# Optimization experiments

Measured on AMD Instinct MI355X. Metric: run time of the kernel, lower is better.

Reference implementation:

```python
import jax, jax.numpy as jnp
import numpy as np

B, CIN, H, W = 16, 512, 64, 64
CP = 256  # planes
G = 8     # groups
EPS = 1e-5


def setup_inputs() -> dict:
    key = jax.random.key(0)
    ks = jax.random.split(key, 7)
    s_in = 1.0 / np.sqrt(CIN)
    s_zp = 1.0 / np.sqrt(CP // G)
    return {
        "x": jax.random.normal(ks[0], (B, CIN, H, W), dtype=jnp.float32),
        "Wt": jax.random.uniform(ks[1], (CP, CIN), jnp.float32, -s_in, s_in),
        "Wp": jax.random.uniform(ks[2], (CP, CIN), jnp.float32, -s_in, s_in),
        "Wg": jax.random.uniform(ks[3], (CP, CIN), jnp.float32, -s_in, s_in),
        # grouped 1x1 conv z: (groups, out_per_group=CIN//G, in_per_group=CP//G)
        "Wz": jax.random.uniform(ks[4], (G, CIN // G, CP // G), jnp.float32, -s_zp, s_zp),
        "gamma": jnp.ones((CIN,), jnp.float32),
        "beta": jnp.zeros((CIN,), jnp.float32),
    }


def reference(x, Wt, Wp, Wg, Wz, gamma, beta):
    b, cin, h, w = x.shape
    cp = Wt.shape[0]
    cg = cp // G  # channels per group in bottleneck
    n = cg * h * w

    # 1x1 convs == channel matmuls
    t = jnp.einsum("oi,bihw->bohw", Wt, x)
    p = jnp.einsum("oi,bihw->bohw", Wp, x)
    g = jnp.einsum("oi,bihw->bohw", Wg, x)

    # per-group CGNL dot-product kernel: att = <p_g, g_g> (scalar), y = att * t_g
    t = t.reshape(b, G, n)
    p = p.reshape(b, G, n)
    g = g.reshape(b, G, n)
    att = jnp.sum(p * g, axis=-1, keepdims=True)  # (b, G, 1); use_scale=False
    y = (att * t).reshape(b, G, cg, h * w)

    # grouped 1x1 conv z back to cin channels
    z = jnp.einsum("goc,bgcn->bgon", Wz, y).reshape(b, cin, h, w)

    # GroupNorm(G, cin) + residual
    zr = z.reshape(b, G, (cin // G) * h * w)
    mu = jnp.mean(zr, axis=-1, keepdims=True)
    var = jnp.var(zr, axis=-1, keepdims=True)
    zn = ((zr - mu) * jax.lax.rsqrt(var + EPS)).reshape(b, cin, h, w)
    out = zn * gamma[None, :, None, None] + beta[None, :, None, None] + x
    return out
```

## Files before the change

### kernel.cpp

```cpp
#include <hip/hip_runtime.h>
#include <stddef.h>
#include <stdint.h>

#define B_   16
#define CIN_ 512
#define HW_  4096
#define CP_  256
#define G_   8
#define EPS_ 1e-5f

typedef _Float16 f16;
typedef _Float16 f16x8 __attribute__((ext_vector_type(8)));
typedef _Float16 f16x2 __attribute__((ext_vector_type(2)));
typedef float    f32x4 __attribute__((ext_vector_type(4)));

#define OFF_WALL   0u
#define OFF_WZH    786432u
#define OFF_ATT    819200u
#define OFF_STATS  819712u
#define OFF_T      1048576u
#define OFF_XH     34603008u

#if defined(__has_builtin)
#if __has_builtin(__builtin_amdgcn_fdot2)
#define HAVE_FDOT2 1
#endif
#endif

__device__ __forceinline__ float dot2acc(f16x2 a, f16x2 b, float c) {
#ifdef HAVE_FDOT2
  return __builtin_amdgcn_fdot2(a, b, c, false);
#else
  return fmaf((float)a[0], (float)b[0], fmaf((float)a[1], (float)b[1], c));
#endif
}

__global__ __launch_bounds__(256) void k_prep0(
    const float* __restrict__ Wt, const float* __restrict__ Wp,
    const float* __restrict__ Wg, const float* __restrict__ Wz,
    char* __restrict__ ws)
{
  f16*   wall  = (f16*)(ws + OFF_WALL);
  f16*   wzh   = (f16*)(ws + OFF_WZH);
  float* att   = (float*)(ws + OFF_ATT);
  int idx = blockIdx.x * 256 + threadIdx.x;
  if (idx < 768 * 512) {
    int r = idx >> 9, k = idx & 511;
    float v;
    if (r < 256) v = Wt[r * 512 + k];
    else {
      int q = r - 256, o = q >> 1;
      v = (q & 1) ? Wg[o * 512 + k] : Wp[o * 512 + k];
    }
    wall[idx] = (f16)v;
  } else if (idx < 768 * 512 + 16384) {
    int i = idx - 768 * 512;
    wzh[i] = (f16)Wz[i];
  } else if (idx < 768 * 512 + 16384 + 384) {
    att[idx - (768 * 512 + 16384)] = 0.f;
  }
}

__global__ __launch_bounds__(256) void k_xpose(const float* __restrict__ x,
                                               f16* __restrict__ xh)
{
  __shared__ f16 T[64][72];
  const int tid = threadIdx.x;
  const int c0  = blockIdx.x * 64;
  const int hw0 = blockIdx.y * 64;
  const int b   = blockIdx.z;

  const int cr  = (tid >> 4) * 4;
  const int hwr = (tid & 15) * 4;
  const float* xb = x + ((size_t)b * CIN_ + c0) * HW_ + hw0;

  float4 v[4];
#pragma unroll
  for (int j = 0; j < 4; j++)
    v[j] = *(const float4*)(xb + (size_t)(cr + j) * HW_ + hwr);

#pragma unroll
  for (int i = 0; i < 4; i++) {
    f16 pk[4];
#pragma unroll
    for (int j = 0; j < 4; j++) pk[j] = (f16)((const float*)&v[j])[i];
    *(f16x2*)&T[hwr + i][cr]     = f16x2{pk[0], pk[1]};
    *(f16x2*)&T[hwr + i][cr + 2] = f16x2{pk[2], pk[3]};
  }
  __syncthreads();

  const int hwo = tid >> 2;
  const int cb  = (tid & 3) * 16;
  f16* dst = xh + ((size_t)b * HW_ + hw0 + hwo) * 512 + c0 + cb;
  *(f16x8*)(dst)     = *(const f16x8*)&T[hwo][cb];
  *(f16x8*)(dst + 8) = *(const f16x8*)&T[hwo][cb + 8];
}

__global__ __launch_bounds__(256) void k_gemm(
    const f16* __restrict__ xh, const f16* __restrict__ wall,
    f16* __restrict__ tbuf, float* __restrict__ att, int bchunk)
{
  __shared__ f16 As[128 * 64];
  __shared__ f16 Bs[128 * 64];

  const int tid = threadIdx.x;
  const int bid = blockIdx.x;
  const int logical = (bid & 7) * 96 + (bid >> 3);
  const int nt = logical % 6;
  const int mt = (logical / 6) & 31;
  const int bl = logical / 192;
  const int M0 = mt * 128;
  const int N0 = nt * 128;

  const int l  = tid & 63;
  const int w  = tid >> 6;
  const int wy = w >> 1, wx = w & 1;

  const f16* xb = xh + (size_t)bl * HW_ * 512;

  f32x4 acc[4][4] = {};

  const int srow  = tid >> 3;
  const int sslot = tid & 7;
  const unsigned ldsW = (unsigned)(w * 1024);

  for (int k0 = 0; k0 < 512; k0 += 64) {
    __syncthreads();
#pragma unroll
    for (int i = 0; i < 4; i++) {
      const int r  = srow + i * 32;
      const int sl = sslot ^ (r & 7);
      const f16* ga = xb + (size_t)(M0 + r) * 512 + k0 + sl * 8;
      __builtin_amdgcn_global_load_lds(
          (const __attribute__((address_space(1))) void*)ga,
          (__attribute__((address_space(3))) void*)((char*)As + i * 4096 + ldsW),
          16, 0, 0);
      const f16* gb = wall + (size_t)(N0 + r) * 512 + k0 + sl * 8;
      __builtin_amdgcn_global_load_lds(
          (const __attribute__((address_space(1))) void*)gb,
          (__attribute__((address_space(3))) void*)((char*)Bs + i * 4096 + ldsW),
          16, 0, 0);
    }
    __syncthreads();

#pragma unroll
    for (int ks = 0; ks < 2; ks++) {
      f16x8 af[4], bf[4];
#pragma unroll
      for (int f = 0; f < 4; f++) {
        const int ra = wy * 64 + f * 16 + (l & 15);
        const int sa = (ks * 4 + (l >> 4)) ^ (ra & 7);
        af[f] = *(const f16x8*)&As[ra * 64 + sa * 8];
        const int rb = wx * 64 + f * 16 + (l & 15);
        const int sb = (ks * 4 + (l >> 4)) ^ (rb & 7);
        bf[f] = *(const f16x8*)&Bs[rb * 64 + sb * 8];
      }
#pragma unroll
      for (int fi = 0; fi < 4; fi++)
#pragma unroll
        for (int fj = 0; fj < 4; fj++)
          acc[fi][fj] = __builtin_amdgcn_mfma_f32_16x16x32_f16(
              af[fi], bf[fj], acc[fi][fj], 0, 0, 0);
    }
  }

  const int bg = bchunk + bl;
  if (N0 < 256) {
    f16* tb = tbuf + (size_t)bg * HW_ * 256;
#pragma unroll
    for (int fi = 0; fi < 4; fi++) {
      const int hwr = M0 + wy * 64 + fi * 16 + (l >> 4) * 4;
#pragma unroll
      for (int fj = 0; fj < 4; fj++) {
        const int c = N0 + wx * 64 + fj * 16 + (l & 15);
#pragma unroll
        for (int r = 0; r < 4; r++)
          tb[(size_t)(hwr + r) * 256 + c] = (f16)acc[fi][fj][r];
      }
    }
  } else {
    float s = 0.f;
#pragma unroll
    for (int fi = 0; fi < 4; fi++)
#pragma unroll
      for (int fj = 0; fj < 4; fj++)
#pragma unroll
        for (int r = 0; r < 4; r++) {
          const float v = acc[fi][fj][r];
          s += v * __shfl_xor(v, 1);
        }
#pragma unroll
    for (int off = 32; off > 0; off >>= 1) s += __shfl_xor(s, off);
    if (l == 0) {
      const int grp = (N0 + wx * 64 - 256) >> 6;
      atomicAdd(&att[bg * G_ + grp], 0.5f * s);
    }
  }
}

__global__ __launch_bounds__(256) void k_stats(
    const f16* __restrict__ tbuf, const f16* __restrict__ wzh,
    float* __restrict__ stats)
{
  __shared__ f16x2 wzs[64 * 16];
  __shared__ float red[8];
  const int tid = threadIdx.x;
  const int n0 = blockIdx.x * 1024;
  const int g  = blockIdx.y;
  const int b  = blockIdx.z;

  ((uint4*)wzs)[tid] = ((const uint4*)(wzh + (size_t)g * 2048))[tid];
  __syncthreads();

  const f16* tb = tbuf + ((size_t)b * HW_ + n0 + tid * 4) * 256 + g * 32;
  f16x8 tv[4][4];
#pragma unroll
  for (int j = 0; j < 4; j++)
#pragma unroll
    for (int q = 0; q < 4; q++)
      tv[j][q] = *(const f16x8*)(tb + (size_t)j * 256 + q * 8);

  float s1 = 0.f, s2 = 0.f;
#pragma unroll 2
  for (int o = 0; o < 64; o++) {
    float u[4] = {0.f, 0.f, 0.f, 0.f};
#pragma unroll
    for (int q = 0; q < 4; q++) {
#pragma unroll
      for (int e = 0; e < 4; e++) {
        const f16x2 wz2 = wzs[o * 16 + q * 4 + e];
#pragma unroll
        for (int j = 0; j < 4; j++) {
          const f16x2 t2 = {tv[j][q][2 * e], tv[j][q][2 * e + 1]};
          u[j] = dot2acc(wz2, t2, u[j]);
        }
      }
    }
#pragma unroll
    for (int j = 0; j < 4; j++) {
      s1 += u[j];
      s2 = fmaf(u[j], u[j], s2);
    }
  }
#pragma unroll
  for (int off = 32; off > 0; off >>= 1) {
    s1 += __shfl_xor(s1, off);
    s2 += __shfl_xor(s2, off);
  }
  if ((tid & 63) == 0) { red[(tid >> 6) * 2] = s1; red[(tid >> 6) * 2 + 1] = s2; }
  __syncthreads();
  if (tid == 0) {
    atomicAdd(&stats[(b * G_ + g) * 2 + 0], red[0] + red[2] + red[4] + red[6]);
    atomicAdd(&stats[(b * G_ + g) * 2 + 1], red[1] + red[3] + red[5] + red[7]);
  }
}

__global__ __launch_bounds__(256) void k_out(
    const f16* __restrict__ tbuf, const f16* __restrict__ wzh,
    const float* __restrict__ x, const float* __restrict__ gamma,
    const float* __restrict__ beta, const float* __restrict__ att,
    const float* __restrict__ stats, float* __restrict__ out)
{
  __shared__ f16x2 wzs[64 * 16];
  const int tid = threadIdx.x;
  const int n0 = blockIdx.x * 1024;
  const int g  = blockIdx.y;
  const int b  = blockIdx.z;

  ((uint4*)wzs)[tid] = ((const uint4*)(wzh + (size_t)g * 2048))[tid];
  __syncthreads();

  const f16* tb = tbuf + ((size_t)b * HW_ + n0 + tid * 4) * 256 + g * 32;
  f16x8 tv[4][4];
#pragma unroll
  for (int j = 0; j < 4; j++)
#pragma unroll
    for (int q = 0; q < 4; q++)
      tv[j][q] = *(const f16x8*)(tb + (size_t)j * 256 + q * 8);

  const float attv = att[b * G_ + g];
  const float invN = 1.f / (64.f * 4096.f);
  const float S1 = stats[(b * G_ + g) * 2 + 0];
  const float S2 = stats[(b * G_ + g) * 2 + 1];
  const float mu  = S1 * invN;
  const float var = S2 * invN - mu * mu;
  const float sc  = attv * rsqrtf(attv * attv * var + EPS_);

#pragma unroll 2
  for (int o = 0; o < 64; o++) {
    float u[4] = {0.f, 0.f, 0.f, 0.f};
#pragma unroll
    for (int q = 0; q < 4; q++) {
#pragma unroll
      for (int e = 0; e < 4; e++) {
        const f16x2 wz2 = wzs[o * 16 + q * 4 + e];
#pragma unroll
        for (int j = 0; j < 4; j++) {
          const f16x2 t2 = {tv[j][q][2 * e], tv[j][q][2 * e + 1]};
          u[j] = dot2acc(wz2, t2, u[j]);
        }
      }
    }
    const int c = g * 64 + o;
    const float gm = gamma[c];
    const float bt = beta[c];
    const size_t off = ((size_t)b * CIN_ + c) * HW_ + n0 + tid * 4;
    const float4 xv = *(const float4*)(x + off);
    float4 ov;
    ov.x = fmaf((u[0] - mu) * sc, gm, bt + xv.x);
    ov.y = fmaf((u[1] - mu) * sc, gm, bt + xv.y);
    ov.z = fmaf((u[2] - mu) * sc, gm, bt + xv.z);
    ov.w = fmaf((u[3] - mu) * sc, gm, bt + xv.w);
    *(float4*)(out + off) = ov;
  }
}

extern "C" void kernel_launch(void* const* d_in, const int* in_sizes, int n_in,
                              void* d_out, int out_size, void* d_ws, size_t ws_size,
                              hipStream_t stream)
{
  const float* x     = (const float*)d_in[0];
  const float* Wt    = (const float*)d_in[1];
  const float* Wp    = (const float*)d_in[2];
  const float* Wg    = (const float*)d_in[3];
  const float* Wz    = (const float*)d_in[4];
  const float* gamma = (const float*)d_in[5];
  const float* beta  = (const float*)d_in[6];
  float* out = (float*)d_out;

  char* ws = (char*)d_ws;
  f16*   wall  = (f16*)(ws + OFF_WALL);
  f16*   wzh   = (f16*)(ws + OFF_WZH);
  float* att   = (float*)(ws + OFF_ATT);
  float* stats = (float*)(ws + OFF_STATS);
  f16*   tbuf  = (f16*)(ws + OFF_T);
  f16*   xh    = (f16*)(ws + OFF_XH);

  k_prep0<<<1602, 256, 0, stream>>>(Wt, Wp, Wg, Wz, ws);

  for (int cb = 0; cb < 4; cb++) {
    dim3 gx(8, 64, 4);
    k_xpose<<<gx, 256, 0, stream>>>(x + (size_t)cb * 4 * CIN_ * HW_, xh);
    k_gemm<<<768, 256, 0, stream>>>(xh, wall, tbuf, att, cb * 4);
  }

  dim3 g2(4, G_, B_);
  k_stats<<<g2, 256, 0, stream>>>(tbuf, wzh, stats);
  k_out<<<g2, 256, 0, stream>>>(tbuf, wzh, x, gamma, beta, att, stats, out);
}
```

Before: 456.5 us.

## Merge batch-chunk launches and stage GEMM epilogue through LDS for vector stores

```diff
diff --git a/kernel.cpp b/kernel.cpp
--- a/kernel.cpp
+++ b/kernel.cpp
@@ -98,17 +98,20 @@
 
 __global__ __launch_bounds__(256) void k_gemm(
     const f16* __restrict__ xh, const f16* __restrict__ wall,
-    f16* __restrict__ tbuf, float* __restrict__ att, int bchunk)
-{
-  __shared__ f16 As[128 * 64];
-  __shared__ f16 Bs[128 * 64];
+    f16* __restrict__ tbuf, float* __restrict__ att)
+{
+  __shared__ union SM {
+    struct { f16 A[128 * 64]; f16 B[128 * 64]; } s;
+    f16 ep[4][64 * 72];
+  } sm;
 
   const int tid = threadIdx.x;
   const int bid = blockIdx.x;
-  const int logical = (bid & 7) * 96 + (bid >> 3);
-  const int nt = logical % 6;
-  const int mt = (logical / 6) & 31;
-  const int bl = logical / 192;
+  const int logical = (bid & 7) * 384 + (bid >> 3);
+  const int nt   = logical % 6;
+  const int rest = logical / 6;
+  const int mt   = rest & 31;
+  const int bl   = rest >> 5;
   const int M0 = mt * 128;
   const int N0 = nt * 128;
 
@@ -133,12 +136,12 @@
       const f16* ga = xb + (size_t)(M0 + r) * 512 + k0 + sl * 8;
       __builtin_amdgcn_global_load_lds(
           (const __attribute__((address_space(1))) void*)ga,
-          (__attribute__((address_space(3))) void*)((char*)As + i * 4096 + ldsW),
+          (__attribute__((address_space(3))) void*)((char*)sm.s.A + i * 4096 + ldsW),
           16, 0, 0);
       const f16* gb = wall + (size_t)(N0 + r) * 512 + k0 + sl * 8;
       __builtin_amdgcn_global_load_lds(
           (const __attribute__((address_space(1))) void*)gb,
-          (__attribute__((address_space(3))) void*)((char*)Bs + i * 4096 + ldsW),
+          (__attribute__((address_space(3))) void*)((char*)sm.s.B + i * 4096 + ldsW),
           16, 0, 0);
     }
     __syncthreads();
@@ -150,10 +153,10 @@
       for (int f = 0; f < 4; f++) {
         const int ra = wy * 64 + f * 16 + (l & 15);
         const int sa = (ks * 4 + (l >> 4)) ^ (ra & 7);
-        af[f] = *(const f16x8*)&As[ra * 64 + sa * 8];
+        af[f] = *(const f16x8*)&sm.s.A[ra * 64 + sa * 8];
         const int rb = wx * 64 + f * 16 + (l & 15);
         const int sb = (ks * 4 + (l >> 4)) ^ (rb & 7);
-        bf[f] = *(const f16x8*)&Bs[rb * 64 + sb * 8];
+        bf[f] = *(const f16x8*)&sm.s.B[rb * 64 + sb * 8];
       }
 #pragma unroll
       for (int fi = 0; fi < 4; fi++)
@@ -164,19 +167,27 @@
     }
   }
 
-  const int bg = bchunk + bl;
+  __syncthreads();
+
   if (N0 < 256) {
-    f16* tb = tbuf + (size_t)bg * HW_ * 256;
-#pragma unroll
-    for (int fi = 0; fi < 4; fi++) {
-      const int hwr = M0 + wy * 64 + fi * 16 + (l >> 4) * 4;
-#pragma unroll
-      for (int fj = 0; fj < 4; fj++) {
-        const int c = N0 + wx * 64 + fj * 16 + (l & 15);
+    f16* ep = sm.ep[w];
+#pragma unroll
+    for (int fi = 0; fi < 4; fi++)
+#pragma unroll
+      for (int fj = 0; fj < 4; fj++)
 #pragma unroll
         for (int r = 0; r < 4; r++)
-          tb[(size_t)(hwr + r) * 256 + c] = (f16)acc[fi][fj][r];
-      }
+          ep[(fi * 16 + (l >> 4) * 4 + r) * 72 + fj * 16 + (l & 15)] =
+              (f16)acc[fi][fj][r];
+    f16* tb = tbuf + (size_t)bl * HW_ * 256;
+    const int hwb = M0 + wy * 64;
+    const int cb2 = N0 + wx * 64;
+#pragma unroll
+    for (int q = 0; q < 8; q++) {
+      const int row = q * 8 + (l >> 3);
+      const int cc  = (l & 7) * 8;
+      *(f16x8*)&tb[(size_t)(hwb + row) * 256 + cb2 + cc] =
+          *(const f16x8*)&ep[row * 72 + cc];
     }
   } else {
     float s = 0.f;
@@ -193,7 +204,7 @@
     for (int off = 32; off > 0; off >>= 1) s += __shfl_xor(s, off);
     if (l == 0) {
       const int grp = (N0 + wx * 64 - 256) >> 6;
-      atomicAdd(&att[bg * G_ + grp], 0.5f * s);
+      atomicAdd(&att[bl * G_ + grp], 0.5f * s);
     }
   }
 }
@@ -338,11 +349,9 @@
 
   k_prep0<<<1602, 256, 0, stream>>>(Wt, Wp, Wg, Wz, ws);
 
-  for (int cb = 0; cb < 4; cb++) {
-    dim3 gx(8, 64, 4);
-    k_xpose<<<gx, 256, 0, stream>>>(x + (size_t)cb * 4 * CIN_ * HW_, xh);
-    k_gemm<<<768, 256, 0, stream>>>(xh, wall, tbuf, att, cb * 4);
-  }
+  dim3 gx(8, 64, 16);
+  k_xpose<<<gx, 256, 0, stream>>>(x, xh);
+  k_gemm<<<3072, 256, 0, stream>>>(xh, wall, tbuf, att);
 
   dim3 g2(4, G_, B_);
   k_stats<<<g2, 256, 0, stream>>>(tbuf, wzh, stats);
```

New measurement: 394.8 us. 1.16x faster.
